# Kernel optimization log

Hardware: AMD Instinct MI355X
Metric: run time of the kernel (lower is better)

The kernel has to match this reference:

```python
import jax, jax.numpy as jnp
import numpy as np

C_IN = 256
A = 2086
H_BOARD, W_BOARD = 10, 9
S = H_BOARD * W_BOARD  # 90
E = 2                  # embed dim after 1x1 conv
NH = 2                 # num attention heads (head_dim = 1)
B = 4096
BN_EPS = 1e-5


def setup_inputs() -> dict:
    key = jax.random.key(0)
    ks = jax.random.split(key, 12)
    inp = {
        "x": jax.random.normal(ks[0], (B, C_IN, H_BOARD, W_BOARD), dtype=jnp.float32),
        # 1x1 conv, no bias: weight [out=2, in=256]
        "conv_w": jax.random.normal(ks[1], (E, C_IN), dtype=jnp.float32) * 0.05,
        # BatchNorm2d(2) params / running stats (inference-mode BN)
        "bn_gamma": jnp.ones((E,), dtype=jnp.float32),
        "bn_beta": jnp.zeros((E,), dtype=jnp.float32),
        "bn_mean": jax.random.normal(ks[2], (E,), dtype=jnp.float32) * 0.1,
        "bn_var": jax.random.uniform(ks[3], (E,), dtype=jnp.float32, minval=0.5, maxval=1.5),
        # MultiheadAttention packed in-proj: [3*E, E], bias [3*E]
        "in_proj_w": jax.random.normal(ks[4], (3 * E, E), dtype=jnp.float32) * 0.5,
        "in_proj_b": jax.random.normal(ks[5], (3 * E,), dtype=jnp.float32) * 0.05,
        "out_proj_w": jax.random.normal(ks[6], (E, E), dtype=jnp.float32) * 0.5,
        "out_proj_b": jax.random.normal(ks[7], (E,), dtype=jnp.float32) * 0.05,
        # Linear(2*90 -> 2086)
        "fc_w": jax.random.normal(ks[8], (A, E * S), dtype=jnp.float32) * 0.05,
        "fc_b": jax.random.normal(ks[9], (A,), dtype=jnp.float32) * 0.05,
    }
    return inp


def reference(x, conv_w, bn_gamma, bn_beta, bn_mean, bn_var,
              in_proj_w, in_proj_b, out_proj_w, out_proj_b, fc_w, fc_b):
    b = x.shape[0]
    # 1x1 conv (bias-free) == channel contraction: [b,256,h,w] -> [b,2,h,w]
    y = jnp.einsum('bchw,oc->bohw', x, conv_w)
    # BatchNorm2d (inference): (y - mean) / sqrt(var + eps) * gamma + beta
    scale = (bn_gamma * jax.lax.rsqrt(bn_var + BN_EPS))[None, :, None, None]
    shift = (bn_beta - bn_mean * bn_gamma * jax.lax.rsqrt(bn_var + BN_EPS))[None, :, None, None]
    y = y * scale + shift
    # [b,2,h,w] -> [b, S, 2]  (seq = board cells, feature = 2 channels)
    xf = y.reshape(b, E, S).transpose(0, 2, 1)
    # packed QKV projection
    qkv = xf @ in_proj_w.T + in_proj_b          # [b,S,3E]
    q, k, v = jnp.split(qkv, 3, axis=-1)        # each [b,S,E]
    hd = E // NH                                 # head_dim = 1
    def split_heads(t):
        return t.reshape(b, S, NH, hd).transpose(0, 2, 1, 3)  # [b,nh,S,hd]
    q, k, v = split_heads(q), split_heads(k), split_heads(v)
    scores = jnp.einsum('bhqd,bhkd->bhqk', q, k) / jnp.sqrt(jnp.float32(hd))
    attn = jax.nn.softmax(scores, axis=-1)      # [b,nh,S,S]
    o = jnp.einsum('bhqk,bhkd->bhqd', attn, v)  # [b,nh,S,hd]
    o = o.transpose(0, 2, 1, 3).reshape(b, S, E)
    o = o @ out_proj_w.T + out_proj_b           # [b,S,E]
    # [b,S,E] -> [b,E,S] -> [b, E*S], matching permute(0,2,1).view(b,-1)
    flat = o.transpose(0, 2, 1).reshape(b, E * S)
    logits = flat @ fc_w.T + fc_b               # [b, 2086]
    return logits
```

## Files before the change

kernel.cpp:

```cpp
#include <hip/hip_runtime.h>

#define C_IN    256
#define S_CELLS 90
#define A_OUT   2086
#define K_FC    180
#define K_PAD   192
#define N_PAD   2176
#define B_BATCH 4096

typedef __attribute__((ext_vector_type(8))) short short8;
typedef __attribute__((ext_vector_type(4))) float floatx4;

static __device__ __forceinline__ unsigned short f2bf(float f) {
    unsigned u = __float_as_uint(f);
    return (unsigned short)((u + 0x7FFFu + ((u >> 16) & 1u)) >> 16);
}

__global__ __launch_bounds__(512) void front_kernel(
    const float* __restrict__ x,
    const float* __restrict__ conv_w,
    const float* __restrict__ bn_gamma,
    const float* __restrict__ bn_beta,
    const float* __restrict__ bn_mean,
    const float* __restrict__ bn_var,
    const float* __restrict__ ipw,
    const float* __restrict__ ipb,
    const float* __restrict__ opw,
    const float* __restrict__ opb,
    unsigned short* __restrict__ Abf)
{
    __shared__ float4 kvs[8][S_CELLS];

    const int wid  = threadIdx.x >> 6;
    const int lane = threadIdx.x & 63;
    const int b    = blockIdx.x * 8 + wid;

    float qA0 = 0.f, qA1 = 0.f, qB0 = 0.f, qB1 = 0.f;
    const int sA = 2 * lane;
    const int sB = 2 * lane + 1;

    if (lane < 45) {
        const float2* xb2 = reinterpret_cast<const float2*>(
                                x + (size_t)b * (C_IN * S_CELLS)) + lane;
        float a00 = 0.f, a01 = 0.f, a10 = 0.f, a11 = 0.f;
        #pragma unroll 8
        for (int c = 0; c < C_IN; ++c) {
            const float2 v = xb2[c * 45];
            const float w0 = conv_w[c];
            const float w1 = conv_w[C_IN + c];
            a00 = fmaf(w0, v.x, a00); a01 = fmaf(w0, v.y, a01);
            a10 = fmaf(w1, v.x, a10); a11 = fmaf(w1, v.y, a11);
        }
        const float sc0 = bn_gamma[0] * rsqrtf(bn_var[0] + 1e-5f);
        const float sc1 = bn_gamma[1] * rsqrtf(bn_var[1] + 1e-5f);
        const float sh0 = bn_beta[0] - bn_mean[0] * sc0;
        const float sh1 = bn_beta[1] - bn_mean[1] * sc1;
        const float yA0 = a00 * sc0 + sh0, yA1 = a10 * sc1 + sh1;
        const float yB0 = a01 * sc0 + sh0, yB1 = a11 * sc1 + sh1;

        qA0 = ipw[0] * yA0 + ipw[1] * yA1 + ipb[0];
        qA1 = ipw[2] * yA0 + ipw[3] * yA1 + ipb[1];
        qB0 = ipw[0] * yB0 + ipw[1] * yB1 + ipb[0];
        qB1 = ipw[2] * yB0 + ipw[3] * yB1 + ipb[1];

        kvs[wid][sA] = make_float4(
            ipw[4] * yA0 + ipw[5]  * yA1 + ipb[2],
            ipw[8] * yA0 + ipw[9]  * yA1 + ipb[4],
            ipw[6] * yA0 + ipw[7]  * yA1 + ipb[3],
            ipw[10]* yA0 + ipw[11] * yA1 + ipb[5]);
        kvs[wid][sB] = make_float4(
            ipw[4] * yB0 + ipw[5]  * yB1 + ipb[2],
            ipw[8] * yB0 + ipw[9]  * yB1 + ipb[4],
            ipw[6] * yB0 + ipw[7]  * yB1 + ipb[3],
            ipw[10]* yB0 + ipw[11] * yB1 + ipb[5]);
    }
    __syncthreads();

    if (lane < 45) {
        float dA0 = 0.f, nA0 = 0.f, dA1 = 0.f, nA1 = 0.f;
        float dB0 = 0.f, nB0 = 0.f, dB1 = 0.f, nB1 = 0.f;
        #pragma unroll 5
        for (int j = 0; j < S_CELLS; ++j) {
            const float4 kv = kvs[wid][j];
            float e;
            e = __expf(qA0 * kv.x); dA0 += e; nA0 = fmaf(e, kv.y, nA0);
            e = __expf(qA1 * kv.z); dA1 += e; nA1 = fmaf(e, kv.w, nA1);
            e = __expf(qB0 * kv.x); dB0 += e; nB0 = fmaf(e, kv.y, nB0);
            e = __expf(qB1 * kv.z); dB1 += e; nB1 = fmaf(e, kv.w, nB1);
        }
        const float oA0 = nA0 / dA0, oA1 = nA1 / dA1;
        const float oB0 = nB0 / dB0, oB1 = nB1 / dB1;
        unsigned short* ab = Abf + (size_t)b * K_PAD;
        ab[sA]           = f2bf(opw[0] * oA0 + opw[1] * oA1 + opb[0]);
        ab[S_CELLS + sA] = f2bf(opw[2] * oA0 + opw[3] * oA1 + opb[1]);
        ab[sB]           = f2bf(opw[0] * oB0 + opw[1] * oB1 + opb[0]);
        ab[S_CELLS + sB] = f2bf(opw[2] * oB0 + opw[3] * oB1 + opb[1]);
    } else if (lane < 57) {
        Abf[(size_t)b * K_PAD + 135 + lane] = 0;
    }
}

#define BM 128
#define BN 128
#define BK 64
#define LDSROW 72

__global__ __launch_bounds__(256) void fc_mfma_kernel(
    const unsigned short* __restrict__ Abf,
    const float* __restrict__ W,
    const float* __restrict__ bias,
    float* __restrict__ out)
{
    __shared__ __align__(16) unsigned short As[BM * LDSROW];
    __shared__ __align__(16) unsigned short Bs[BN * LDSROW];

    const int tid  = threadIdx.x;
    const int lane = tid & 63;
    const int wave = tid >> 6;
    const int wy   = wave >> 1;
    const int wx   = wave & 1;
    const int lrow = lane & 15;
    const int lk   = (lane >> 4) * 8;
    const int bm   = blockIdx.y * BM;
    const int bn   = blockIdx.x * BN;

    floatx4 acc[4][4] = {};

    for (int k0 = 0; k0 < K_PAD; k0 += BK) {
        for (int q = tid; q < BM * 8; q += 256) {
            const int m = q >> 3, c = q & 7;
            *(int4*)&As[m * LDSROW + c * 8] =
                *(const int4*)(Abf + (size_t)(bm + m) * K_PAD + k0 + c * 8);

            const int n  = bn + m;
            const int kb = k0 + c * 8;
            unsigned short h[8];
            if (n < A_OUT && kb + 7 < K_FC) {
                const float4 f0 = *(const float4*)(W + (size_t)n * K_FC + kb);
                const float4 f1 = *(const float4*)(W + (size_t)n * K_FC + kb + 4);
                h[0] = f2bf(f0.x); h[1] = f2bf(f0.y); h[2] = f2bf(f0.z); h[3] = f2bf(f0.w);
                h[4] = f2bf(f1.x); h[5] = f2bf(f1.y); h[6] = f2bf(f1.z); h[7] = f2bf(f1.w);
            } else {
                #pragma unroll
                for (int t = 0; t < 8; ++t) {
                    const int k = kb + t;
                    h[t] = (n < A_OUT && k < K_FC)
                           ? f2bf(W[(size_t)n * K_FC + k]) : (unsigned short)0;
                }
            }
            *(int4*)&Bs[m * LDSROW + c * 8] = *(const int4*)h;
        }
        __syncthreads();

        #pragma unroll
        for (int ks = 0; ks < 2; ++ks) {
            short8 af[4], bf[4];
            #pragma unroll
            for (int t = 0; t < 4; ++t) {
                af[t] = *(const short8*)&As[(wy * 64 + t * 16 + lrow) * LDSROW + ks * 32 + lk];
                bf[t] = *(const short8*)&Bs[(wx * 64 + t * 16 + lrow) * LDSROW + ks * 32 + lk];
            }
            #pragma unroll
            for (int mt = 0; mt < 4; ++mt)
                #pragma unroll
                for (int nt = 0; nt < 4; ++nt)
                    acc[mt][nt] = __builtin_amdgcn_mfma_f32_16x16x32_bf16(
                        af[mt], bf[nt], acc[mt][nt], 0, 0, 0);
        }
        __syncthreads();
    }

    const int ccol = lane & 15;
    const int crow = (lane >> 4) * 4;
    #pragma unroll
    for (int mt = 0; mt < 4; ++mt) {
        #pragma unroll
        for (int nt = 0; nt < 4; ++nt) {
            const int n_out = bn + wx * 64 + nt * 16 + ccol;
            if (n_out >= A_OUT) continue;
            const int m_base = bm + wy * 64 + mt * 16 + crow;
            const float bv = bias[n_out];
            #pragma unroll
            for (int r = 0; r < 4; ++r)
                out[(size_t)(m_base + r) * A_OUT + n_out] = acc[mt][nt][r] + bv;
        }
    }
}

extern "C" void kernel_launch(void* const* d_in, const int* in_sizes, int n_in,
                              void* d_out, int out_size, void* d_ws, size_t ws_size,
                              hipStream_t stream) {
    const float* x        = (const float*)d_in[0];
    const float* conv_w   = (const float*)d_in[1];
    const float* bn_gamma = (const float*)d_in[2];
    const float* bn_beta  = (const float*)d_in[3];
    const float* bn_mean  = (const float*)d_in[4];
    const float* bn_var   = (const float*)d_in[5];
    const float* ipw      = (const float*)d_in[6];
    const float* ipb      = (const float*)d_in[7];
    const float* opw      = (const float*)d_in[8];
    const float* opb      = (const float*)d_in[9];
    const float* fc_w     = (const float*)d_in[10];
    const float* fc_b     = (const float*)d_in[11];
    float* out = (float*)d_out;

    unsigned short* Abf = (unsigned short*)d_ws;

    front_kernel<<<dim3(B_BATCH / 8), 512, 0, stream>>>(
        x, conv_w, bn_gamma, bn_beta, bn_mean, bn_var,
        ipw, ipb, opw, opb, Abf);

    fc_mfma_kernel<<<dim3(N_PAD / BN, B_BATCH / BM), 256, 0, stream>>>(
        Abf, fc_w, fc_b, out);
}
```

Baseline: 552.1 us.

## Prequantize FC weights in separate kernel, vectorize conv loads, shrink GEMM M-tile

The front kernel now reads the input as float4, so each lane covers four cells across a pair of channels, then combines even and odd channel partials through shared memory. Output stores are packed as 32-bit pairs. A new kernel converts the FC weights to padded bf16 once per call, so the GEMM no longer reconverts fp32 weights in every tile, and the GEMM M-tile drops from 128 to 64 to launch more blocks. The extra launch and the workspace round trip for the bf16 weights are added in exchange.

```diff
diff --git a/kernel.cpp b/kernel.cpp
--- a/kernel.cpp
+++ b/kernel.cpp
@@ -16,7 +16,7 @@
     return (unsigned short)((u + 0x7FFFu + ((u >> 16) & 1u)) >> 16);
 }
 
-__global__ __launch_bounds__(512) void front_kernel(
+__global__ __launch_bounds__(256) void front_kernel(
     const float* __restrict__ x,
     const float* __restrict__ conv_w,
     const float* __restrict__ bn_gamma,
@@ -29,46 +29,75 @@
     const float* __restrict__ opb,
     unsigned short* __restrict__ Abf)
 {
-    __shared__ float4 kvs[8][S_CELLS];
-
-    const int wid  = threadIdx.x >> 6;
+    __shared__ float2 part[4][2 * S_CELLS];
+    __shared__ float4 kvs[4][S_CELLS];
+
+    const int wv   = threadIdx.x >> 6;
     const int lane = threadIdx.x & 63;
-    const int b    = blockIdx.x * 8 + wid;
+    const int b    = blockIdx.x * 4 + wv;
+
+    if (lane < 45) {
+        const float4* xb4 = reinterpret_cast<const float4*>(
+                                x + (size_t)b * (C_IN * S_CELLS)) + lane;
+        const float2* w0p = reinterpret_cast<const float2*>(conv_w);
+        const float2* w1p = reinterpret_cast<const float2*>(conv_w + C_IN);
+        const int e0 = 4 * lane;
+        const bool o0 = (e0 + 0) >= S_CELLS;
+        const bool o1 = (e0 + 1) >= S_CELLS;
+        const bool o2 = (e0 + 2) >= S_CELLS;
+        const bool o3 = (e0 + 3) >= S_CELLS;
+
+        float a0[4] = {0.f, 0.f, 0.f, 0.f};
+        float a1[4] = {0.f, 0.f, 0.f, 0.f};
+        #pragma unroll 4
+        for (int cp = 0; cp < C_IN / 2; ++cp) {
+            const float4 v  = xb4[cp * 45];
+            const float2 w0 = w0p[cp];
+            const float2 w1 = w1p[cp];
+            a0[0] = fmaf(o0 ? w0.y : w0.x, v.x, a0[0]);
+            a1[0] = fmaf(o0 ? w1.y : w1.x, v.x, a1[0]);
+            a0[1] = fmaf(o1 ? w0.y : w0.x, v.y, a0[1]);
+            a1[1] = fmaf(o1 ? w1.y : w1.x, v.y, a1[1]);
+            a0[2] = fmaf(o2 ? w0.y : w0.x, v.z, a0[2]);
+            a1[2] = fmaf(o2 ? w1.y : w1.x, v.z, a1[2]);
+            a0[3] = fmaf(o3 ? w0.y : w0.x, v.w, a0[3]);
+            a1[3] = fmaf(o3 ? w1.y : w1.x, v.w, a1[3]);
+        }
+        part[wv][e0 + 0] = make_float2(a0[0], a1[0]);
+        part[wv][e0 + 1] = make_float2(a0[1], a1[1]);
+        part[wv][e0 + 2] = make_float2(a0[2], a1[2]);
+        part[wv][e0 + 3] = make_float2(a0[3], a1[3]);
+    }
+    __syncthreads();
 
     float qA0 = 0.f, qA1 = 0.f, qB0 = 0.f, qB1 = 0.f;
     const int sA = 2 * lane;
     const int sB = 2 * lane + 1;
 
     if (lane < 45) {
-        const float2* xb2 = reinterpret_cast<const float2*>(
-                                x + (size_t)b * (C_IN * S_CELLS)) + lane;
-        float a00 = 0.f, a01 = 0.f, a10 = 0.f, a11 = 0.f;
-        #pragma unroll 8
-        for (int c = 0; c < C_IN; ++c) {
-            const float2 v = xb2[c * 45];
-            const float w0 = conv_w[c];
-            const float w1 = conv_w[C_IN + c];
-            a00 = fmaf(w0, v.x, a00); a01 = fmaf(w0, v.y, a01);
-            a10 = fmaf(w1, v.x, a10); a11 = fmaf(w1, v.y, a11);
-        }
+        const float2 peA = part[wv][sA], poA = part[wv][S_CELLS + sA];
+        const float2 peB = part[wv][sB], poB = part[wv][S_CELLS + sB];
+
         const float sc0 = bn_gamma[0] * rsqrtf(bn_var[0] + 1e-5f);
         const float sc1 = bn_gamma[1] * rsqrtf(bn_var[1] + 1e-5f);
         const float sh0 = bn_beta[0] - bn_mean[0] * sc0;
         const float sh1 = bn_beta[1] - bn_mean[1] * sc1;
-        const float yA0 = a00 * sc0 + sh0, yA1 = a10 * sc1 + sh1;
-        const float yB0 = a01 * sc0 + sh0, yB1 = a11 * sc1 + sh1;
+        const float yA0 = (peA.x + poA.x) * sc0 + sh0;
+        const float yA1 = (peA.y + poA.y) * sc1 + sh1;
+        const float yB0 = (peB.x + poB.x) * sc0 + sh0;
+        const float yB1 = (peB.y + poB.y) * sc1 + sh1;
 
         qA0 = ipw[0] * yA0 + ipw[1] * yA1 + ipb[0];
         qA1 = ipw[2] * yA0 + ipw[3] * yA1 + ipb[1];
         qB0 = ipw[0] * yB0 + ipw[1] * yB1 + ipb[0];
         qB1 = ipw[2] * yB0 + ipw[3] * yB1 + ipb[1];
 
-        kvs[wid][sA] = make_float4(
+        kvs[wv][sA] = make_float4(
             ipw[4] * yA0 + ipw[5]  * yA1 + ipb[2],
             ipw[8] * yA0 + ipw[9]  * yA1 + ipb[4],
             ipw[6] * yA0 + ipw[7]  * yA1 + ipb[3],
             ipw[10]* yA0 + ipw[11] * yA1 + ipb[5]);
-        kvs[wid][sB] = make_float4(
+        kvs[wv][sB] = make_float4(
             ipw[4] * yB0 + ipw[5]  * yB1 + ipb[2],
             ipw[8] * yB0 + ipw[9]  * yB1 + ipb[4],
             ipw[6] * yB0 + ipw[7]  * yB1 + ipb[3],
@@ -81,7 +110,7 @@
         float dB0 = 0.f, nB0 = 0.f, dB1 = 0.f, nB1 = 0.f;
         #pragma unroll 5
         for (int j = 0; j < S_CELLS; ++j) {
-            const float4 kv = kvs[wid][j];
+            const float4 kv = kvs[wv][j];
             float e;
             e = __expf(qA0 * kv.x); dA0 += e; nA0 = fmaf(e, kv.y, nA0);
             e = __expf(qA1 * kv.z); dA1 += e; nA1 = fmaf(e, kv.w, nA1);
@@ -91,23 +120,35 @@
         const float oA0 = nA0 / dA0, oA1 = nA1 / dA1;
         const float oB0 = nB0 / dB0, oB1 = nB1 / dB1;
         unsigned short* ab = Abf + (size_t)b * K_PAD;
-        ab[sA]           = f2bf(opw[0] * oA0 + opw[1] * oA1 + opb[0]);
-        ab[S_CELLS + sA] = f2bf(opw[2] * oA0 + opw[3] * oA1 + opb[1]);
-        ab[sB]           = f2bf(opw[0] * oB0 + opw[1] * oB1 + opb[0]);
-        ab[S_CELLS + sB] = f2bf(opw[2] * oB0 + opw[3] * oB1 + opb[1]);
+        const unsigned r0A = f2bf(opw[0] * oA0 + opw[1] * oA1 + opb[0]);
+        const unsigned r0B = f2bf(opw[0] * oB0 + opw[1] * oB1 + opb[0]);
+        const unsigned r1A = f2bf(opw[2] * oA0 + opw[3] * oA1 + opb[1]);
+        const unsigned r1B = f2bf(opw[2] * oB0 + opw[3] * oB1 + opb[1]);
+        *(unsigned*)&ab[sA]           = r0A | (r0B << 16);
+        *(unsigned*)&ab[S_CELLS + sA] = r1A | (r1B << 16);
     } else if (lane < 57) {
         Abf[(size_t)b * K_PAD + 135 + lane] = 0;
     }
 }
 
-#define BM 128
+__global__ __launch_bounds__(192) void wconv_kernel(
+    const float* __restrict__ W, unsigned short* __restrict__ Wbf)
+{
+    const int n = blockIdx.x;
+    const int k = threadIdx.x;
+    unsigned short v = 0;
+    if (n < A_OUT && k < K_FC) v = f2bf(W[(size_t)n * K_FC + k]);
+    Wbf[(size_t)n * K_PAD + k] = v;
+}
+
+#define BM 64
 #define BN 128
 #define BK 64
 #define LDSROW 72
 
 __global__ __launch_bounds__(256) void fc_mfma_kernel(
     const unsigned short* __restrict__ Abf,
-    const float* __restrict__ W,
+    const unsigned short* __restrict__ Wbf,
     const float* __restrict__ bias,
     float* __restrict__ out)
 {
@@ -124,44 +165,32 @@
     const int bm   = blockIdx.y * BM;
     const int bn   = blockIdx.x * BN;
 
-    floatx4 acc[4][4] = {};
+    floatx4 acc[2][4] = {};
 
     for (int k0 = 0; k0 < K_PAD; k0 += BK) {
         for (int q = tid; q < BM * 8; q += 256) {
             const int m = q >> 3, c = q & 7;
             *(int4*)&As[m * LDSROW + c * 8] =
                 *(const int4*)(Abf + (size_t)(bm + m) * K_PAD + k0 + c * 8);
-
-            const int n  = bn + m;
-            const int kb = k0 + c * 8;
-            unsigned short h[8];
-            if (n < A_OUT && kb + 7 < K_FC) {
-                const float4 f0 = *(const float4*)(W + (size_t)n * K_FC + kb);
-                const float4 f1 = *(const float4*)(W + (size_t)n * K_FC + kb + 4);
-                h[0] = f2bf(f0.x); h[1] = f2bf(f0.y); h[2] = f2bf(f0.z); h[3] = f2bf(f0.w);
-                h[4] = f2bf(f1.x); h[5] = f2bf(f1.y); h[6] = f2bf(f1.z); h[7] = f2bf(f1.w);
-            } else {
-                #pragma unroll
-                for (int t = 0; t < 8; ++t) {
-                    const int k = kb + t;
-                    h[t] = (n < A_OUT && k < K_FC)
-                           ? f2bf(W[(size_t)n * K_FC + k]) : (unsigned short)0;
-                }
-            }
-            *(int4*)&Bs[m * LDSROW + c * 8] = *(const int4*)h;
+        }
+        for (int q = tid; q < BN * 8; q += 256) {
+            const int m = q >> 3, c = q & 7;
+            *(int4*)&Bs[m * LDSROW + c * 8] =
+                *(const int4*)(Wbf + (size_t)(bn + m) * K_PAD + k0 + c * 8);
         }
         __syncthreads();
 
         #pragma unroll
         for (int ks = 0; ks < 2; ++ks) {
-            short8 af[4], bf[4];
-            #pragma unroll
-            for (int t = 0; t < 4; ++t) {
-                af[t] = *(const short8*)&As[(wy * 64 + t * 16 + lrow) * LDSROW + ks * 32 + lk];
+            short8 af[2], bf[4];
+            #pragma unroll
+            for (int t = 0; t < 2; ++t)
+                af[t] = *(const short8*)&As[(wy * 32 + t * 16 + lrow) * LDSROW + ks * 32 + lk];
+            #pragma unroll
+            for (int t = 0; t < 4; ++t)
                 bf[t] = *(const short8*)&Bs[(wx * 64 + t * 16 + lrow) * LDSROW + ks * 32 + lk];
-            }
-            #pragma unroll
-            for (int mt = 0; mt < 4; ++mt)
+            #pragma unroll
+            for (int mt = 0; mt < 2; ++mt)
                 #pragma unroll
                 for (int nt = 0; nt < 4; ++nt)
                     acc[mt][nt] = __builtin_amdgcn_mfma_f32_16x16x32_bf16(
@@ -173,12 +202,12 @@
     const int ccol = lane & 15;
     const int crow = (lane >> 4) * 4;
     #pragma unroll
-    for (int mt = 0; mt < 4; ++mt) {
+    for (int mt = 0; mt < 2; ++mt) {
         #pragma unroll
         for (int nt = 0; nt < 4; ++nt) {
             const int n_out = bn + wx * 64 + nt * 16 + ccol;
             if (n_out >= A_OUT) continue;
-            const int m_base = bm + wy * 64 + mt * 16 + crow;
+            const int m_base = bm + wy * 32 + mt * 16 + crow;
             const float bv = bias[n_out];
             #pragma unroll
             for (int r = 0; r < 4; ++r)
@@ -205,11 +234,14 @@
     float* out = (float*)d_out;
 
     unsigned short* Abf = (unsigned short*)d_ws;
-
-    front_kernel<<<dim3(B_BATCH / 8), 512, 0, stream>>>(
+    unsigned short* Wbf = (unsigned short*)((char*)d_ws + (size_t)B_BATCH * K_PAD * 2);
+
+    front_kernel<<<dim3(B_BATCH / 4), 256, 0, stream>>>(
         x, conv_w, bn_gamma, bn_beta, bn_mean, bn_var,
         ipw, ipb, opw, opb, Abf);
 
+    wconv_kernel<<<dim3(N_PAD), 192, 0, stream>>>(fc_w, Wbf);
+
     fc_mfma_kernel<<<dim3(N_PAD / BN, B_BATCH / BM), 256, 0, stream>>>(
-        Abf, fc_w, fc_b, out);
-}
+        Abf, Wbf, fc_b, out);
+}
```

New measurement: 561.0 us. Within noise of the previous version (+1.6%).
